# Kernel tuning notes

Hardware: AMD Instinct MI355X
Metric: run time of the kernel (lower is better)

Reference implementation:

```python
import math
import jax, jax.numpy as jnp
import numpy as np

N_HEADS = 12
D_EMBED = 768
BATCH = 2
SEQ = 2048


def setup_inputs() -> dict:
    key = jax.random.key(0)
    ks = jax.random.split(key, 5)
    scale = 0.02
    return {
        "x": jax.random.normal(ks[0], (BATCH, SEQ, D_EMBED), dtype=jnp.float32),
        "w_in": jax.random.normal(ks[1], (D_EMBED, 3 * D_EMBED), dtype=jnp.float32) * scale,
        "b_in": jax.random.normal(ks[2], (3 * D_EMBED,), dtype=jnp.float32) * scale,
        "w_out": jax.random.normal(ks[3], (D_EMBED, D_EMBED), dtype=jnp.float32) * scale,
        "b_out": jax.random.normal(ks[4], (D_EMBED,), dtype=jnp.float32) * scale,
    }


def reference(x, w_in, b_in, w_out, b_out):
    # x: [B, S, D]
    B, S, D = x.shape
    H = N_HEADS
    dh = D // H
    # Fused QKV projection: [B, S, 3D]
    qkv = x @ w_in + b_in
    q, k, v = jnp.split(qkv, 3, axis=-1)
    # [B, S, D] -> [B, H, S, dh]
    def to_heads(t):
        return t.reshape(B, S, H, dh).transpose(0, 2, 1, 3)
    q, k, v = to_heads(q), to_heads(k), to_heads(v)
    # Scaled dot-product attention (non-causal, masked=False default)
    scale = 1.0 / math.sqrt(dh)
    scores = jnp.einsum("bhqd,bhkd->bhqk", q, k) * scale  # [B, H, S, S]
    probs = jax.nn.softmax(scores, axis=-1)
    out = jnp.einsum("bhqk,bhkd->bhqd", probs, v)  # [B, H, S, dh]
    # Merge heads: [B, S, D]
    out = out.transpose(0, 2, 1, 3).reshape(B, S, D)
    return out @ w_out + b_out
```

## Files before the change

### kernel.cpp

```cpp
#include <hip/hip_runtime.h>
#include <stdint.h>

#define B_   2
#define S_   2048
#define D_   768
#define H_   12
#define DH_  64
#define N3_  2304
#define M_   4096

typedef __attribute__((ext_vector_type(8))) short    bf16x8;
typedef __attribute__((ext_vector_type(4))) float    f32x4;
typedef __attribute__((ext_vector_type(4))) int      i32x4;
typedef __attribute__((ext_vector_type(4))) unsigned short u16x4;
typedef _Float16 f16x4 __attribute__((ext_vector_type(4)));
typedef __fp16   h16x2 __attribute__((ext_vector_type(2)));

#define KSCALE 0.18033688011112042f
#define LSTRIDE (24 * S_)
#define ONE_EL  ((size_t)24 * S_ * DH_)

__device__ inline unsigned short f2bf(float f) {
    union { float f; unsigned u; } v; v.f = f;
    unsigned r = v.u + 0x7FFFu + ((v.u >> 16) & 1u);
    return (unsigned short)(r >> 16);
}

__device__ inline void async_copy16(const void* g, void* l) {
    __builtin_amdgcn_global_load_lds((const __attribute__((address_space(1))) void*)g,
                                     (__attribute__((address_space(3))) void*)l, 16, 0, 0);
}

__global__ __launch_bounds__(256) void prep_all(
    const float* __restrict__ x, const float* __restrict__ w_in,
    const float* __restrict__ w_out,
    unsigned short* __restrict__ xb, unsigned short* __restrict__ winT,
    unsigned short* __restrict__ woutT)
{
    __shared__ unsigned short t[32][33];
    const int gid = blockIdx.x, tid = threadIdx.x;
    if (gid < 3072) {
        int i = gid * 256 + tid;
        f32x4 v = *(const f32x4*)(x + (size_t)i * 4);
        u16x4 o;
        o.x = f2bf(v.x); o.y = f2bf(v.y); o.z = f2bf(v.z); o.w = f2bf(v.w);
        *(u16x4*)(xb + (size_t)i * 4) = o;
        return;
    }
    const float* src; unsigned short* dst; int R, C, bx, by;
    if (gid < 4800) { int b = gid - 3072; src = w_in;  dst = winT;  R = D_; C = N3_; bx = b % 72; by = b / 72; }
    else            { int b = gid - 4800; src = w_out; dst = woutT; R = D_; C = D_;  bx = b % 24; by = b / 24; }
    int c0 = bx * 32, r0 = by * 32, tx = tid & 31, ty = tid >> 5;
#pragma unroll
    for (int j = 0; j < 4; j++)
        t[ty + j * 8][tx] = f2bf(src[(size_t)(r0 + ty + j * 8) * C + c0 + tx]);
    __syncthreads();
#pragma unroll
    for (int j = 0; j < 4; j++)
        dst[(size_t)(c0 + ty + j * 8) * R + r0 + tx] = t[tx][ty + j * 8];
}

__global__ __launch_bounds__(256) void gemm_qkv(
    const unsigned short* __restrict__ A,
    const unsigned short* __restrict__ Bt,
    const float* __restrict__ bias,
    unsigned short* __restrict__ QK,
    unsigned short* __restrict__ Vt)
{
    __shared__ __align__(16) short Al[128 * 64];
    __shared__ __align__(16) short Bl[96 * 64];

    const int tid  = threadIdx.x;
    const int w    = tid >> 6;
    const int lane = tid & 63;
    const int r    = lane & 15;
    const int quad = lane >> 4;
    const int bid  = blockIdx.x;
    const int rest = bid >> 3;
    const int m0   = ((bid & 7) + 8 * (rest / 24)) * 128;
    const int n0   = (rest % 24) * 96;
    const int wm   = (w & 1) * 64;
    const int wn   = (w >> 1) * 48;
    const int K    = D_;

    f32x4 acc[4][3];
#pragma unroll
    for (int i = 0; i < 4; i++)
#pragma unroll
        for (int j = 0; j < 3; j++) acc[i][j] = f32x4{0.f, 0.f, 0.f, 0.f};

    size_t ga[4], gb[3];
#pragma unroll
    for (int j = 0; j < 4; j++) {
        int c = tid + 256 * j, row = c >> 3, ch = c & 7, g = ch ^ (row & 7);
        ga[j] = (size_t)(m0 + row) * K + g * 8;
    }
#pragma unroll
    for (int j = 0; j < 3; j++) {
        int c = tid + 256 * j, row = c >> 3, ch = c & 7, g = ch ^ (row & 7);
        gb[j] = (size_t)(n0 + row) * K + g * 8;
    }

    for (int k0 = 0; k0 < K; k0 += 64) {
        __syncthreads();
#pragma unroll
        for (int j = 0; j < 4; j++)
            async_copy16(A + ga[j] + k0, &Al[(j * 256 + w * 64) * 8]);
#pragma unroll
        for (int j = 0; j < 3; j++)
            async_copy16(Bt + gb[j] + k0, &Bl[(j * 256 + w * 64) * 8]);
        __syncthreads();

#pragma unroll
        for (int kk = 0; kk < 2; kk++) {
            bf16x8 af[4], bf[3];
#pragma unroll
            for (int mi = 0; mi < 4; mi++)
                af[mi] = *(const bf16x8*)&Al[(wm + mi * 16 + r) * 64 +
                                             ((kk * 4 + quad) ^ (r & 7)) * 8];
#pragma unroll
            for (int ni = 0; ni < 3; ni++)
                bf[ni] = *(const bf16x8*)&Bl[(wn + ni * 16 + r) * 64 +
                                             ((kk * 4 + quad) ^ (r & 7)) * 8];
#pragma unroll
            for (int mi = 0; mi < 4; mi++)
#pragma unroll
                for (int ni = 0; ni < 3; ni++)
                    acc[mi][ni] = __builtin_amdgcn_mfma_f32_16x16x32_bf16(
                        af[mi], bf[ni], acc[mi][ni], 0, 0, 0);
        }
    }

    const size_t one = (size_t)B_ * H_ * S_ * DH_;
#pragma unroll
    for (int ni = 0; ni < 3; ni++) {
        int col  = n0 + wn + ni * 16 + r;
        float bv = bias[col];
        int part = col / 768;
        int cc   = col - part * 768;
        int h    = cc >> 6;
        int d    = cc & 63;
        if (part == 2) {
#pragma unroll
            for (int mi = 0; mi < 4; mi++) {
                int row0 = m0 + wm + mi * 16 + quad * 4;
                int b    = row0 >> 11;
                int s0   = row0 & 2047;
                u16x4 pk;
#pragma unroll
                for (int i = 0; i < 4; i++) {
                    union { _Float16 h; unsigned short s; } cv;
                    cv.h = (_Float16)(acc[mi][ni][i] + bv);
                    pk[i] = cv.s;
                }
                *(u16x4*)&Vt[(((size_t)(b * H_ + h)) * DH_ + d) * S_ + s0] = pk;
            }
        } else {
            float scl = (part == 1) ? KSCALE : 1.0f;
            unsigned short* dst = QK + (size_t)part * one;
#pragma unroll
            for (int mi = 0; mi < 4; mi++) {
#pragma unroll
                for (int i = 0; i < 4; i++) {
                    int row = m0 + wm + mi * 16 + quad * 4 + i;
                    int b   = row >> 11;
                    int s   = row & 2047;
                    dst[(((size_t)(b * H_ + h)) * S_ + s) * DH_ + d] =
                        f2bf((acc[mi][ni][i] + bv) * scl);
                }
            }
        }
    }
}

__global__ __launch_bounds__(256) void gemm_out(
    const unsigned short* __restrict__ A,
    const unsigned short* __restrict__ Bt,
    const float* __restrict__ bias,
    float* __restrict__ Cf)
{
    __shared__ __align__(16) short Al[2][64 * 64];
    __shared__ __align__(16) short Bl[2][64 * 64];

    const int tid  = threadIdx.x;
    const int w    = tid >> 6;
    const int lane = tid & 63;
    const int r    = lane & 15;
    const int quad = lane >> 4;
    const int bid  = blockIdx.x;
    const int rest = bid >> 3;
    const int m0   = ((bid & 7) + 8 * (rest / 12)) * 64;
    const int n0   = (rest % 12) * 64;
    const int wm   = (w & 1) * 32;
    const int wn   = (w >> 1) * 32;
    const int K    = D_;
    const int N    = D_;

    f32x4 acc[2][2];
#pragma unroll
    for (int i = 0; i < 2; i++)
#pragma unroll
        for (int j = 0; j < 2; j++) acc[i][j] = f32x4{0.f, 0.f, 0.f, 0.f};

    size_t ga[2], gb[2];
#pragma unroll
    for (int j = 0; j < 2; j++) {
        int c = tid + 256 * j, row = c >> 3, ch = c & 7, g = ch ^ (row & 7);
        ga[j] = (size_t)(m0 + row) * K + g * 8;
        gb[j] = (size_t)(n0 + row) * K + g * 8;
    }

#pragma unroll
    for (int j = 0; j < 2; j++) {
        async_copy16(A  + ga[j], &Al[0][(j * 256 + w * 64) * 8]);
        async_copy16(Bt + gb[j], &Bl[0][(j * 256 + w * 64) * 8]);
    }
    __syncthreads();

    for (int it = 0; it < 12; it++) {
        const int cur = it & 1;
        if (it < 11) {
            const int k0 = (it + 1) * 64;
#pragma unroll
            for (int j = 0; j < 2; j++) {
                async_copy16(A  + ga[j] + k0, &Al[cur ^ 1][(j * 256 + w * 64) * 8]);
                async_copy16(Bt + gb[j] + k0, &Bl[cur ^ 1][(j * 256 + w * 64) * 8]);
            }
        }
#pragma unroll
        for (int kk = 0; kk < 2; kk++) {
            bf16x8 af[2], bf[2];
#pragma unroll
            for (int mi = 0; mi < 2; mi++)
                af[mi] = *(const bf16x8*)&Al[cur][(wm + mi * 16 + r) * 64 +
                                                  ((kk * 4 + quad) ^ (r & 7)) * 8];
#pragma unroll
            for (int ni = 0; ni < 2; ni++)
                bf[ni] = *(const bf16x8*)&Bl[cur][(wn + ni * 16 + r) * 64 +
                                                  ((kk * 4 + quad) ^ (r & 7)) * 8];
#pragma unroll
            for (int mi = 0; mi < 2; mi++)
#pragma unroll
                for (int ni = 0; ni < 2; ni++)
                    acc[mi][ni] = __builtin_amdgcn_mfma_f32_16x16x32_bf16(
                        af[mi], bf[ni], acc[mi][ni], 0, 0, 0);
        }
        __syncthreads();
    }

#pragma unroll
    for (int ni = 0; ni < 2; ni++) {
        int col  = n0 + wn + ni * 16 + r;
        float bv = bias[col];
#pragma unroll
        for (int mi = 0; mi < 2; mi++) {
#pragma unroll
            for (int i = 0; i < 4; i++) {
                int row = m0 + wm + mi * 16 + quad * 4 + i;
                Cf[(size_t)row * N + col] = acc[mi][ni][i] + bv;
            }
        }
    }
}

__global__ __launch_bounds__(256) void attn_kernel(
    const unsigned short* __restrict__ Q,
    const unsigned short* __restrict__ K,
    const unsigned short* __restrict__ Vt,
    unsigned short* __restrict__ On,
    float* __restrict__ lbuf)
{
    __shared__ __align__(16) short Kl[64 * 64];
    __shared__ __align__(16) short Vl[64 * 64];

    const int tid  = threadIdx.x;
    const int w    = tid >> 6;
    const int lane = tid & 63;
    const int r    = lane & 15;
    const int quad = lane >> 4;
    const int xk   = r & 7;
    const int bid  = blockIdx.x;
    const int bh   = bid % 24;
    const int t2   = bid / 24;
    const int qb   = t2 & 15;
    const int half = t2 >> 4;
    const size_t baseQK = (size_t)bh * S_ * DH_;
    const size_t baseV  = (size_t)bh * DH_ * S_;
    const int q0   = qb * 128;
    const int kt0  = half * 16;

    bf16x8 qf[2][2];
#pragma unroll
    for (int qt = 0; qt < 2; qt++) {
        const unsigned short* qp =
            Q + baseQK + (size_t)(q0 + w * 32 + qt * 16 + r) * DH_ + quad * 8;
        qf[qt][0] = *(const bf16x8*)(qp);
        qf[qt][1] = *(const bf16x8*)(qp + 32);
    }

    f32x4 o[2][4];
    f32x4 lacc[2];
#pragma unroll
    for (int qt = 0; qt < 2; qt++) {
        lacc[qt] = f32x4{0.f, 0.f, 0.f, 0.f};
#pragma unroll
        for (int nb = 0; nb < 4; nb++) o[qt][nb] = f32x4{0.f, 0.f, 0.f, 0.f};
    }

    const f16x4 ONES = {(_Float16)1.f, (_Float16)1.f, (_Float16)1.f, (_Float16)1.f};

    const int srw = tid >> 3, schk = tid & 7;
    const unsigned short* kg = K  + baseQK + (size_t)kt0 * 4096 + tid * 8;
    const unsigned short* vg = Vt + baseV + (size_t)kt0 * 64 + (size_t)srw * S_ + schk * 8;
    const int lb = srw * 64 + (schk ^ (srw & 7)) * 8;

    i32x4 kreg[2], vreg[2];
    kreg[0] = *(const i32x4*)(kg);
    kreg[1] = *(const i32x4*)(kg + 2048);
    vreg[0] = *(const i32x4*)(vg);
    vreg[1] = *(const i32x4*)(vg + 32 * S_);

    for (int it = 0; it < 16; it++) {
        __syncthreads();
        *(i32x4*)&Kl[lb]        = kreg[0];
        *(i32x4*)&Kl[lb + 2048] = kreg[1];
        *(i32x4*)&Vl[lb]        = vreg[0];
        *(i32x4*)&Vl[lb + 2048] = vreg[1];
        __syncthreads();

        if (it != 15) {
            const unsigned short* kn = kg + (it + 1) * 4096;
            const unsigned short* vn = vg + (it + 1) * 64;
            kreg[0] = *(const i32x4*)(kn);
            kreg[1] = *(const i32x4*)(kn + 2048);
            vreg[0] = *(const i32x4*)(vn);
            vreg[1] = *(const i32x4*)(vn + 32 * S_);
        }

        f32x4 sa[2][4];
#pragma unroll
        for (int qt = 0; qt < 2; qt++)
#pragma unroll
            for (int kb = 0; kb < 4; kb++) sa[qt][kb] = f32x4{0.f, 0.f, 0.f, 0.f};
#pragma unroll
        for (int t = 0; t < 2; t++)
#pragma unroll
            for (int kb = 0; kb < 4; kb++) {
                bf16x8 kf = *(const bf16x8*)&Kl[(kb * 16 + r) * 64 + ((t * 4 + quad) ^ xk) * 8];
#pragma unroll
                for (int qt = 0; qt < 2; qt++)
                    sa[qt][kb] = __builtin_amdgcn_mfma_f32_16x16x32_bf16(
                        kf, qf[qt][t], sa[qt][kb], 0, 0, 0);
            }

        f16x4 pf[2][4];
#pragma unroll
        for (int qt = 0; qt < 2; qt++)
#pragma unroll
            for (int kb = 0; kb < 4; kb++) {
                float p0 = __builtin_amdgcn_exp2f(sa[qt][kb][0]);
                float p1 = __builtin_amdgcn_exp2f(sa[qt][kb][1]);
                float p2 = __builtin_amdgcn_exp2f(sa[qt][kb][2]);
                float p3 = __builtin_amdgcn_exp2f(sa[qt][kb][3]);
                union { f16x4 v; h16x2 h[2]; } u;
                u.h[0] = __builtin_amdgcn_cvt_pkrtz(p0, p1);
                u.h[1] = __builtin_amdgcn_cvt_pkrtz(p2, p3);
                pf[qt][kb] = u.v;
            }

#pragma unroll
        for (int kb = 0; kb < 4; kb++) {
#pragma unroll
            for (int nb = 0; nb < 4; nb++) {
                f16x4 vf = *(const f16x4*)&Vl[(nb * 16 + r) * 64 +
                                              ((kb * 2 + (quad >> 1)) ^ xk) * 8 + (quad & 1) * 4];
#pragma unroll
                for (int qt = 0; qt < 2; qt++)
                    o[qt][nb] = __builtin_amdgcn_mfma_f32_16x16x16f16(
                        pf[qt][kb], vf, o[qt][nb], 0, 0, 0);
            }
#pragma unroll
            for (int qt = 0; qt < 2; qt++)
                lacc[qt] = __builtin_amdgcn_mfma_f32_16x16x16f16(
                    pf[qt][kb], ONES, lacc[qt], 0, 0, 0);
        }
    }

    unsigned short* Ob = On + (size_t)half * ONE_EL;
#pragma unroll
    for (int qt = 0; qt < 2; qt++)
#pragma unroll
        for (int i = 0; i < 4; i++) {
            int s = q0 + w * 32 + qt * 16 + quad * 4 + i;
            size_t row = (size_t)bh * S_ + s;
            if (r == 0) lbuf[half * LSTRIDE + row] = lacc[qt][i];
#pragma unroll
            for (int nb = 0; nb < 4; nb++) {
                union { _Float16 h; unsigned short u; } cv;
                cv.h = (_Float16)o[qt][nb][i];
                Ob[row * 64 + nb * 16 + r] = cv.u;
            }
        }
}

__global__ void combine_attn(const unsigned short* __restrict__ On,
                             const float* __restrict__ lbuf,
                             unsigned short* __restrict__ Out)
{
    int g   = blockIdx.x * 256 + threadIdx.x;
    int hd8 = g % 96;
    int bs  = g / 96;
    int h   = hd8 >> 3;
    int d8  = (hd8 & 7) * 8;
    size_t row = ((size_t)((bs >> 11) * H_ + h)) * S_ + (bs & 2047);
    float inv = 1.0f / (lbuf[row] + lbuf[LSTRIDE + row]);
    size_t ob = row * 64 + d8;
    i32x4 a0 = *(const i32x4*)&On[ob];
    i32x4 a1 = *(const i32x4*)&On[ob + ONE_EL];
    const _Float16* f0 = (const _Float16*)&a0;
    const _Float16* f1 = (const _Float16*)&a1;
    unsigned short tmp[8];
#pragma unroll
    for (int j = 0; j < 8; j++)
        tmp[j] = f2bf(((float)f0[j] + (float)f1[j]) * inv);
    *(i32x4*)&Out[(size_t)bs * D_ + h * 64 + d8] = *(const i32x4*)tmp;
}

extern "C" void kernel_launch(void* const* d_in, const int* in_sizes, int n_in,
                              void* d_out, int out_size, void* d_ws, size_t ws_size,
                              hipStream_t stream) {
    const float* x     = (const float*)d_in[0];
    const float* w_in  = (const float*)d_in[1];
    const float* b_in  = (const float*)d_in[2];
    const float* w_out = (const float*)d_in[3];
    const float* b_out = (const float*)d_in[4];
    float* out = (float*)d_out;
    char* ws = (char*)d_ws;

    unsigned short* xb    = (unsigned short*)(ws);
    unsigned short* winT  = (unsigned short*)(ws + 6291456);
    unsigned short* woutT = (unsigned short*)(ws + 9830400);
    unsigned short* QKV   = (unsigned short*)(ws + 11010048);
    unsigned short* On    = (unsigned short*)(ws + 36175872);

    const size_t one = (size_t)B_ * H_ * S_ * DH_;
    unsigned short* Vtbuf = QKV + 2 * one;
    float*          lbuf  = (float*)winT;
    unsigned short* attnO = QKV;

    prep_all<<<5376, 256, 0, stream>>>(x, w_in, w_out, xb, winT, woutT);

    gemm_qkv<<<768, 256, 0, stream>>>(xb, winT, b_in, QKV, Vtbuf);

    attn_kernel<<<24 * 16 * 2, 256, 0, stream>>>(
        QKV, QKV + one, Vtbuf, On, lbuf);

    combine_attn<<<1536, 256, 0, stream>>>(On, lbuf, attnO);

    gemm_out<<<768, 256, 0, stream>>>(attnO, woutT, b_out, out);
}
```

Measured before the change: 152.4 us.

## Double-buffer QKV GEMM shared-memory tiles with K-step of 32

Converts the QKV projection GEMM from single-buffered 64-wide K tiles, with two barriers per step, to double-buffered 32-wide K tiles. The next tile's async copies are issued before the MFMAs on the current tile, leaving one barrier per step. The aim is to overlap global-to-LDS loads with compute and cut synchronization stalls. In exchange it doubles the number of loop iterations and uses a narrower XOR swizzle that may cause more LDS bank conflicts.

```diff
diff --git a/kernel.cpp b/kernel.cpp
--- a/kernel.cpp
+++ b/kernel.cpp
@@ -67,8 +67,8 @@
     unsigned short* __restrict__ QK,
     unsigned short* __restrict__ Vt)
 {
-    __shared__ __align__(16) short Al[128 * 64];
-    __shared__ __align__(16) short Bl[96 * 64];
+    __shared__ __align__(16) short Al[2][128 * 32];
+    __shared__ __align__(16) short Bl[2][96 * 32];
 
     const int tid  = threadIdx.x;
     const int w    = tid >> 6;
@@ -89,46 +89,53 @@
 #pragma unroll
         for (int j = 0; j < 3; j++) acc[i][j] = f32x4{0.f, 0.f, 0.f, 0.f};
 
-    size_t ga[4], gb[3];
-#pragma unroll
-    for (int j = 0; j < 4; j++) {
-        int c = tid + 256 * j, row = c >> 3, ch = c & 7, g = ch ^ (row & 7);
-        ga[j] = (size_t)(m0 + row) * K + g * 8;
-    }
-#pragma unroll
-    for (int j = 0; j < 3; j++) {
-        int c = tid + 256 * j, row = c >> 3, ch = c & 7, g = ch ^ (row & 7);
-        gb[j] = (size_t)(n0 + row) * K + g * 8;
-    }
-
-    for (int k0 = 0; k0 < K; k0 += 64) {
+    size_t ga0, ga1, gb0, gb1;
+    {
+        int c = tid,        row = c >> 2, ch = c & 3, g = ch ^ (row & 3);
+        ga0 = (size_t)(m0 + row) * K + g * 8;
+        gb0 = (size_t)(n0 + row) * K + g * 8;
+    }
+    {
+        int c = tid + 256,  row = c >> 2, ch = c & 3, g = ch ^ (row & 3);
+        ga1 = (size_t)(m0 + row) * K + g * 8;
+        gb1 = (size_t)(n0 + row) * K + g * 8;
+    }
+    short* lA0[2] = { &Al[0][(w * 64) * 8],         &Al[1][(w * 64) * 8] };
+    short* lA1[2] = { &Al[0][(256 + w * 64) * 8],   &Al[1][(256 + w * 64) * 8] };
+    short* lB0[2] = { &Bl[0][(w * 64) * 8],         &Bl[1][(w * 64) * 8] };
+    short* lB1[2] = { &Bl[0][(256 + w * 64) * 8],   &Bl[1][(256 + w * 64) * 8] };
+
+    async_copy16(A  + ga0, lA0[0]);
+    async_copy16(A  + ga1, lA1[0]);
+    async_copy16(Bt + gb0, lB0[0]);
+    if (w < 2) async_copy16(Bt + gb1, lB1[0]);
+    __syncthreads();
+
+    for (int it = 0; it < 24; it++) {
+        const int cur = it & 1;
+        if (it < 23) {
+            const int k0 = (it + 1) * 32;
+            async_copy16(A  + ga0 + k0, lA0[cur ^ 1]);
+            async_copy16(A  + ga1 + k0, lA1[cur ^ 1]);
+            async_copy16(Bt + gb0 + k0, lB0[cur ^ 1]);
+            if (w < 2) async_copy16(Bt + gb1 + k0, lB1[cur ^ 1]);
+        }
+        bf16x8 af[4], bf[3];
+#pragma unroll
+        for (int mi = 0; mi < 4; mi++)
+            af[mi] = *(const bf16x8*)&Al[cur][(wm + mi * 16 + r) * 32 +
+                                             (quad ^ (r & 3)) * 8];
+#pragma unroll
+        for (int ni = 0; ni < 3; ni++)
+            bf[ni] = *(const bf16x8*)&Bl[cur][(wn + ni * 16 + r) * 32 +
+                                             (quad ^ (r & 3)) * 8];
+#pragma unroll
+        for (int mi = 0; mi < 4; mi++)
+#pragma unroll
+            for (int ni = 0; ni < 3; ni++)
+                acc[mi][ni] = __builtin_amdgcn_mfma_f32_16x16x32_bf16(
+                    af[mi], bf[ni], acc[mi][ni], 0, 0, 0);
         __syncthreads();
-#pragma unroll
-        for (int j = 0; j < 4; j++)
-            async_copy16(A + ga[j] + k0, &Al[(j * 256 + w * 64) * 8]);
-#pragma unroll
-        for (int j = 0; j < 3; j++)
-            async_copy16(Bt + gb[j] + k0, &Bl[(j * 256 + w * 64) * 8]);
-        __syncthreads();
-
-#pragma unroll
-        for (int kk = 0; kk < 2; kk++) {
-            bf16x8 af[4], bf[3];
-#pragma unroll
-            for (int mi = 0; mi < 4; mi++)
-                af[mi] = *(const bf16x8*)&Al[(wm + mi * 16 + r) * 64 +
-                                             ((kk * 4 + quad) ^ (r & 7)) * 8];
-#pragma unroll
-            for (int ni = 0; ni < 3; ni++)
-                bf[ni] = *(const bf16x8*)&Bl[(wn + ni * 16 + r) * 64 +
-                                             ((kk * 4 + quad) ^ (r & 7)) * 8];
-#pragma unroll
-            for (int mi = 0; mi < 4; mi++)
-#pragma unroll
-                for (int ni = 0; ni < 3; ni++)
-                    acc[mi][ni] = __builtin_amdgcn_mfma_f32_16x16x32_bf16(
-                        af[mi], bf[ni], acc[mi][ni], 0, 0, 0);
-        }
     }
 
     const size_t one = (size_t)B_ * H_ * S_ * DH_;
```

New measurement: 158.5 us. 4.0% more time.

## Fuse split-KV attention combine into output projection GEMM A-tile load

Applied to the files above, without the earlier changes.

Removes the separate combine_attn kernel and instead merges the two partial attention outputs, normalizes them by the summed denominators, and converts to bf16 while staging the A tile in gemm_out. This eliminates a kernel launch and the round trip of the intermediate bf16 attention output through global memory. In exchange, the A operand now uses synchronous register loads instead of async copies and re-reads two fp16 partial buffers per column block, adding conversion math inside the GEMM loop.

```diff
diff --git a/kernel.cpp b/kernel.cpp
--- a/kernel.cpp
+++ b/kernel.cpp
@@ -174,7 +174,8 @@
 }
 
 __global__ __launch_bounds__(256) void gemm_out(
-    const unsigned short* __restrict__ A,
+    const unsigned short* __restrict__ On,
+    const float* __restrict__ lbuf,
     const unsigned short* __restrict__ Bt,
     const float* __restrict__ bias,
     float* __restrict__ Cf)
@@ -202,29 +203,55 @@
 #pragma unroll
         for (int j = 0; j < 2; j++) acc[i][j] = f32x4{0.f, 0.f, 0.f, 0.f};
 
-    size_t ga[2], gb[2];
+    size_t abase[2]; int lrow0[2];
+    size_t gb[2];
 #pragma unroll
     for (int j = 0; j < 2; j++) {
         int c = tid + 256 * j, row = c >> 3, ch = c & 7, g = ch ^ (row & 7);
-        ga[j] = (size_t)(m0 + row) * K + g * 8;
+        int m = m0 + row, b = m >> 11, s = m & 2047;
+        lrow0[j] = b * (H_ * S_) + s;
+        abase[j] = (size_t)lrow0[j] * 64 + g * 8;
         gb[j] = (size_t)(n0 + row) * K + g * 8;
     }
 
+    auto a_write = [&](int buf, const i32x4* a0, const i32x4* a1,
+                       const float* l0, const float* l1) {
+#pragma unroll
+        for (int j = 0; j < 2; j++) {
+            float inv = 1.0f / (l0[j] + l1[j]);
+            const _Float16* f0 = (const _Float16*)&a0[j];
+            const _Float16* f1 = (const _Float16*)&a1[j];
+            unsigned short t8[8];
+#pragma unroll
+            for (int e = 0; e < 8; e++)
+                t8[e] = f2bf(((float)f0[e] + (float)f1[e]) * inv);
+            *(i32x4*)&Al[buf][(tid + 256 * j) * 8] = *(const i32x4*)t8;
+        }
+    };
+
+    i32x4 a0[2], a1[2]; float l0[2], l1[2];
 #pragma unroll
     for (int j = 0; j < 2; j++) {
-        async_copy16(A  + ga[j], &Al[0][(j * 256 + w * 64) * 8]);
+        a0[j] = *(const i32x4*)&On[abase[j]];
+        a1[j] = *(const i32x4*)&On[abase[j] + ONE_EL];
+        l0[j] = lbuf[lrow0[j]];
+        l1[j] = lbuf[LSTRIDE + lrow0[j]];
         async_copy16(Bt + gb[j], &Bl[0][(j * 256 + w * 64) * 8]);
     }
+    a_write(0, a0, a1, l0, l1);
     __syncthreads();
 
     for (int it = 0; it < 12; it++) {
         const int cur = it & 1;
         if (it < 11) {
-            const int k0 = (it + 1) * 64;
+            const int itn = it + 1;
 #pragma unroll
             for (int j = 0; j < 2; j++) {
-                async_copy16(A  + ga[j] + k0, &Al[cur ^ 1][(j * 256 + w * 64) * 8]);
-                async_copy16(Bt + gb[j] + k0, &Bl[cur ^ 1][(j * 256 + w * 64) * 8]);
+                a0[j] = *(const i32x4*)&On[abase[j] + (size_t)itn * 131072];
+                a1[j] = *(const i32x4*)&On[abase[j] + (size_t)itn * 131072 + ONE_EL];
+                l0[j] = lbuf[lrow0[j] + itn * S_];
+                l1[j] = lbuf[LSTRIDE + lrow0[j] + itn * S_];
+                async_copy16(Bt + gb[j] + itn * 64, &Bl[cur ^ 1][(j * 256 + w * 64) * 8]);
             }
         }
 #pragma unroll
@@ -245,6 +272,7 @@
                     acc[mi][ni] = __builtin_amdgcn_mfma_f32_16x16x32_bf16(
                         af[mi], bf[ni], acc[mi][ni], 0, 0, 0);
         }
+        if (it < 11) a_write(cur ^ 1, a0, a1, l0, l1);
         __syncthreads();
     }
 
@@ -403,29 +431,6 @@
         }
 }
 
-__global__ void combine_attn(const unsigned short* __restrict__ On,
-                             const float* __restrict__ lbuf,
-                             unsigned short* __restrict__ Out)
-{
-    int g   = blockIdx.x * 256 + threadIdx.x;
-    int hd8 = g % 96;
-    int bs  = g / 96;
-    int h   = hd8 >> 3;
-    int d8  = (hd8 & 7) * 8;
-    size_t row = ((size_t)((bs >> 11) * H_ + h)) * S_ + (bs & 2047);
-    float inv = 1.0f / (lbuf[row] + lbuf[LSTRIDE + row]);
-    size_t ob = row * 64 + d8;
-    i32x4 a0 = *(const i32x4*)&On[ob];
-    i32x4 a1 = *(const i32x4*)&On[ob + ONE_EL];
-    const _Float16* f0 = (const _Float16*)&a0;
-    const _Float16* f1 = (const _Float16*)&a1;
-    unsigned short tmp[8];
-#pragma unroll
-    for (int j = 0; j < 8; j++)
-        tmp[j] = f2bf(((float)f0[j] + (float)f1[j]) * inv);
-    *(i32x4*)&Out[(size_t)bs * D_ + h * 64 + d8] = *(const i32x4*)tmp;
-}
-
 extern "C" void kernel_launch(void* const* d_in, const int* in_sizes, int n_in,
                               void* d_out, int out_size, void* d_ws, size_t ws_size,
                               hipStream_t stream) {
@@ -446,7 +451,6 @@
     const size_t one = (size_t)B_ * H_ * S_ * DH_;
     unsigned short* Vtbuf = QKV + 2 * one;
     float*          lbuf  = (float*)winT;
-    unsigned short* attnO = QKV;
 
     prep_all<<<5376, 256, 0, stream>>>(x, w_in, w_out, xb, winT, woutT);
 
@@ -455,7 +459,5 @@
     attn_kernel<<<24 * 16 * 2, 256, 0, stream>>>(
         QKV, QKV + one, Vtbuf, On, lbuf);
 
-    combine_attn<<<1536, 256, 0, stream>>>(On, lbuf, attnO);
-
-    gemm_out<<<768, 256, 0, stream>>>(attnO, woutT, b_out, out);
-}
+    gemm_out<<<768, 256, 0, stream>>>(On, lbuf, woutT, b_out, out);
+}
```

Result: no change. 151.7 us, median of 3 (-0.5%).
